# Performance work log

Hardware: AMD Instinct MI355X
Metric: run time of the kernel (lower is better)

The kernel has to match this reference:

```python
import jax, jax.numpy as jnp
import numpy as np

VOCAB, D_MODEL, N_STATE, H_HEADS, LAYERS = 64, 512, 32, 16, 4
EXPAND = 2
D_INNER = EXPAND * D_MODEL          # 1024
P_HEAD = D_INNER // H_HEADS         # 64
CONV_DIM = D_INNER + 2 * N_STATE    # x, B, C share the depthwise conv
K_CONV = 4
D_IN_PROJ = 2 * D_INNER + 2 * N_STATE + H_HEADS  # z, x, B, C, dt
BATCH, SEQ = 4, 1024
EPS = 1e-5


def rmsnorm(x, w):
    return x * jax.lax.rsqrt(jnp.mean(x * x, axis=-1, keepdims=True) + EPS) * w


def silu(x):
    return x * jax.nn.sigmoid(x)


def causal_depthwise_conv(x, w, b):
    # x: [B,L,C], w: [C,K], b: [C]; causal (left) padding, depthwise groups
    xt = jnp.transpose(x, (0, 2, 1))  # [B,C,L]
    out = jax.lax.conv_general_dilated(xt, w[:, None, :], (1,), [(K_CONV - 1, 0)], feature_group_count=w.shape[0])
    return jnp.transpose(out, (0, 2, 1)) + b


def ssd(xh, dt, A, Bm, Cm, Dp):
    # Mamba2 SSD recurrence. xh [B,L,H,P], dt [B,L,H], A [H], Bm/Cm [B,L,N], Dp [H]
    dA = jnp.exp(dt * A)              # decay per (batch, step, head)
    dtx = dt[..., None] * xh          # [B,L,H,P]

    def step(h, inp):
        dA_t, dtx_t, B_t, C_t = inp
        # h: [B,H,P,N]
        h = dA_t[:, :, None, None] * h + dtx_t[..., None] * B_t[:, None, None, :]
        y = jnp.einsum('bhpn,bn->bhp', h, C_t)
        return h, y

    h0 = jnp.zeros((xh.shape[0], H_HEADS, P_HEAD, N_STATE), xh.dtype)
    _, ys = jax.lax.scan(step, h0, (jnp.moveaxis(dA, 1, 0), jnp.moveaxis(dtx, 1, 0), jnp.moveaxis(Bm, 1, 0), jnp.moveaxis(Cm, 1, 0)))
    return jnp.moveaxis(ys, 0, 1) + xh * Dp[None, None, :, None]


def mamba_block(x, norm_w, W_in, b_in, conv_w, conv_b, dt_bias, A_log, Dp, gnorm_w, W_out, b_out):
    res = x
    u = rmsnorm(x, norm_w)
    zxbcdt = u @ W_in + b_in                                # [B,L,D_IN_PROJ]
    z = zxbcdt[..., :D_INNER]
    xBC = zxbcdt[..., D_INNER:D_INNER + CONV_DIM]
    dt = zxbcdt[..., D_INNER + CONV_DIM:]                   # [B,L,H]
    xBC = silu(causal_depthwise_conv(xBC, conv_w, conv_b))
    xc = xBC[..., :D_INNER]
    Bm = xBC[..., D_INNER:D_INNER + N_STATE]
    Cm = xBC[..., D_INNER + N_STATE:]
    dt = jax.nn.softplus(dt + dt_bias)
    xh = xc.reshape(xc.shape[0], xc.shape[1], H_HEADS, P_HEAD)
    y = ssd(xh, dt, -jnp.exp(A_log), Bm, Cm, Dp)
    y = y.reshape(y.shape[0], y.shape[1], D_INNER)
    y = rmsnorm(y * silu(z), gnorm_w)                       # gated RMSNorm
    return res + y @ W_out + b_out


def forward(input_tokens, emb, norm_w, W_in, b_in, conv_w, conv_b, dt_bias, A_log, D_param, gnorm_w, W_out, b_out, head_w, head_b):
    h = emb[input_tokens]
    for i in range(LAYERS):
        h = mamba_block(h, norm_w[i], W_in[i], b_in[i], conv_w[i], conv_b[i], dt_bias[i], A_log[i], D_param[i], gnorm_w[i], W_out[i], b_out[i])
    return h @ head_w + head_b


def setup_inputs() -> dict:
    key = jax.random.key(0)
    ks = jax.random.split(key, 8)
    s = 0.02
    return {
        'input_tokens': jax.random.randint(ks[0], (BATCH, SEQ), 0, VOCAB),
        'emb': jax.random.normal(ks[1], (VOCAB, D_MODEL), jnp.float32) * s,
        'norm_w': jnp.ones((LAYERS, D_MODEL), jnp.float32),
        'W_in': jax.random.normal(ks[2], (LAYERS, D_MODEL, D_IN_PROJ), jnp.float32) * s,
        'b_in': jnp.zeros((LAYERS, D_IN_PROJ), jnp.float32),
        'conv_w': jax.random.normal(ks[3], (LAYERS, CONV_DIM, K_CONV), jnp.float32) * 0.1,
        'conv_b': jnp.zeros((LAYERS, CONV_DIM), jnp.float32),
        'dt_bias': jnp.tile(jnp.log(jnp.expm1(jnp.linspace(0.001, 0.1, H_HEADS, dtype=jnp.float32))), (LAYERS, 1)),
        'A_log': jnp.tile(jnp.log(jnp.arange(1, H_HEADS + 1, dtype=jnp.float32)), (LAYERS, 1)),
        'D_param': jnp.ones((LAYERS, H_HEADS), jnp.float32),
        'gnorm_w': jnp.ones((LAYERS, D_INNER), jnp.float32),
        'W_out': jax.random.normal(ks[4], (LAYERS, D_INNER, D_MODEL), jnp.float32) * s,
        'b_out': jnp.zeros((LAYERS, D_MODEL), jnp.float32),
        'head_w': jax.random.normal(ks[5], (D_MODEL, VOCAB), jnp.float32) * s,
        'head_b': jnp.zeros((VOCAB,), jnp.float32),
    }


def reference(input_tokens, emb, norm_w, W_in, b_in, conv_w, conv_b, dt_bias, A_log, D_param, gnorm_w, W_out, b_out, head_w, head_b):
    return forward(input_tokens, emb, norm_w, W_in, b_in, conv_w, conv_b, dt_bias, A_log, D_param, gnorm_w, W_out, b_out, head_w, head_b)
```

## Files before the change

### kernel.cpp

```cpp
#include <hip/hip_runtime.h>
#include <hip/hip_bf16.h>

#define VOCAB     64
#define D_MODEL   512
#define N_STATE   32
#define H_HEADS   16
#define LAYERS    4
#define D_INNER   1024
#define P_HEAD    64
#define CONV_DIM  1088
#define K_CONV    4
#define D_IN_PROJ 2128
#define NPAD_IN   2176
#define NPAD_HEAD 64
#define BATCH     4
#define SEQ       1024
#define NTOK      (BATCH*SEQ)
#define EPS       1e-5f
#define CL        64
#define NC        (SEQ/CL)
#define PSTR      80

typedef __bf16 bf16x8 __attribute__((ext_vector_type(8)));
typedef float  f32x4  __attribute__((ext_vector_type(4)));

__device__ __forceinline__ float sigmoidf_(float x) { return 1.f / (1.f + __expf(-x)); }
__device__ __forceinline__ float softplusf_(float x) { return (x > 20.f) ? x : log1pf(__expf(x)); }

__device__ __forceinline__ void gload_lds16(const void* g, void* l) {
  __builtin_amdgcn_global_load_lds((const __attribute__((address_space(1))) void*)g,
                                   (__attribute__((address_space(3))) void*)l,
                                   16, 0, 0);
}

__global__ void rmsnorm512_kernel(const float* __restrict__ x, const float* __restrict__ w,
                                  __bf16* __restrict__ out,
                                  const int* __restrict__ tok, const float* __restrict__ emb,
                                  float* __restrict__ hout) {
  int tokid = blockIdx.x;
  int tid = threadIdx.x;
  float v0, v1;
  if (tok) {
    const float* er = emb + (size_t)tok[tokid] * D_MODEL;
    v0 = er[tid]; v1 = er[tid + 256];
    float* hr = hout + (size_t)tokid * D_MODEL;
    hr[tid] = v0; hr[tid + 256] = v1;
  } else {
    const float* xr = x + (size_t)tokid * D_MODEL;
    v0 = xr[tid]; v1 = xr[tid + 256];
  }
  float ss = v0 * v0 + v1 * v1;
  #pragma unroll
  for (int o = 32; o >= 1; o >>= 1) ss += __shfl_xor(ss, o);
  __shared__ float red[4];
  if ((tid & 63) == 0) red[tid >> 6] = ss;
  __syncthreads();
  float tot = red[0] + red[1] + red[2] + red[3];
  float sc = rsqrtf(tot * (1.f / D_MODEL) + EPS);
  out[(size_t)tokid * D_MODEL + tid]       = (__bf16)(v0 * sc * w[tid]);
  out[(size_t)tokid * D_MODEL + tid + 256] = (__bf16)(v1 * sc * w[tid + 256]);
}

__global__ void transpose_cast_kernel(const float* __restrict__ W, __bf16* __restrict__ Wt,
                                      int K, int N, int Npad) {
  W  += (size_t)blockIdx.z * K * N;
  Wt += (size_t)blockIdx.z * Npad * K;
  __shared__ float T[32][33];
  int n0 = blockIdx.x * 32, k0 = blockIdx.y * 32;
  int tx = threadIdx.x & 31, ty = threadIdx.x >> 5;
  #pragma unroll
  for (int i = 0; i < 4; i++) {
    int n = n0 + tx;
    T[ty + i * 8][tx] = (n < N) ? W[(size_t)(k0 + ty + i * 8) * N + n] : 0.f;
  }
  __syncthreads();
  #pragma unroll
  for (int i = 0; i < 4; i++)
    Wt[(size_t)(n0 + ty + i * 8) * K + k0 + tx] = (__bf16)T[tx][ty + i * 8];
}

#define TK 64
__global__ __launch_bounds__(256) void gemm_bf16_kernel(
    const __bf16* __restrict__ A, const __bf16* __restrict__ Bt,
    const float* __restrict__ bias, const float* __restrict__ res,
    float* __restrict__ C, __bf16* __restrict__ Cbf, int K, int N, int ldc) {
  __shared__ __bf16 As[64 * TK];
  __shared__ __bf16 Bs[64 * TK];
  int tid = threadIdx.x;
  int lane = tid & 63, wave = tid >> 6;
  int wm = wave >> 1, wn = wave & 1;
  int q = lane >> 4, l16 = lane & 15;
  size_t row0 = (size_t)blockIdx.y * 64;
  int col0 = blockIdx.x * 64;
  const __bf16* Ab = A + row0 * K;
  const __bf16* Bb = Bt + (size_t)col0 * K;

  f32x4 acc[2][2];
  #pragma unroll
  for (int i = 0; i < 2; i++)
    #pragma unroll
    for (int j = 0; j < 2; j++) acc[i][j] = (f32x4){0.f, 0.f, 0.f, 0.f};

  for (int k0 = 0; k0 < K; k0 += TK) {
    #pragma unroll
    for (int r = 0; r < 2; r++) {
      int lin = r * 256 + tid;
      size_t goff = (size_t)(lin >> 3) * K + k0 + (lin & 7) * 8;
      gload_lds16(Ab + goff, As + lin * 8);
      gload_lds16(Bb + goff, Bs + lin * 8);
    }
    __syncthreads();
    #pragma unroll
    for (int ks = 0; ks < 2; ks++) {
      bf16x8 af[2], bfv[2];
      #pragma unroll
      for (int i = 0; i < 2; i++)
        af[i] = *(const bf16x8*)(As + (wm * 32 + i * 16 + l16) * TK + ks * 32 + q * 8);
      #pragma unroll
      for (int j = 0; j < 2; j++)
        bfv[j] = *(const bf16x8*)(Bs + (wn * 32 + j * 16 + l16) * TK + ks * 32 + q * 8);
      #pragma unroll
      for (int i = 0; i < 2; i++)
        #pragma unroll
        for (int j = 0; j < 2; j++)
          acc[i][j] = __builtin_amdgcn_mfma_f32_16x16x32_bf16(af[i], bfv[j], acc[i][j], 0, 0, 0);
    }
    __syncthreads();
  }

  #pragma unroll
  for (int i = 0; i < 2; i++) {
    size_t mrow = row0 + wm * 32 + i * 16 + q * 4;
    #pragma unroll
    for (int j = 0; j < 2; j++) {
      int col = col0 + wn * 32 + j * 16 + l16;
      if (col < N) {
        float bv = bias ? bias[col] : 0.f;
        #pragma unroll
        for (int rr = 0; rr < 4; rr++) {
          size_t off = (mrow + rr) * (size_t)ldc + col;
          float v = acc[i][j][rr] + bv;
          if (res) v += res[off];
          if (C)   C[off] = v;
          if (Cbf) Cbf[off] = (__bf16)v;
        }
      }
    }
  }
}

__global__ __launch_bounds__(256) void gemm_bf16_128(
    const __bf16* __restrict__ A, const __bf16* __restrict__ Bt,
    const float* __restrict__ bias, __bf16* __restrict__ Cbf,
    int K, int N, int ldc) {
  __shared__ __bf16 As[128 * TK];
  __shared__ __bf16 Bs[128 * TK];
  int tid = threadIdx.x;
  int lane = tid & 63, wave = tid >> 6;
  int wm = wave >> 1, wn = wave & 1;
  int q = lane >> 4, l16 = lane & 15;
  size_t row0 = (size_t)blockIdx.y * 128;
  int col0 = blockIdx.x * 128;
  const __bf16* Ab = A + row0 * K;
  const __bf16* Bb = Bt + (size_t)col0 * K;

  f32x4 acc[4][4];
  #pragma unroll
  for (int i = 0; i < 4; i++)
    #pragma unroll
    for (int j = 0; j < 4; j++) acc[i][j] = (f32x4){0.f, 0.f, 0.f, 0.f};

  for (int k0 = 0; k0 < K; k0 += TK) {
    #pragma unroll
    for (int r = 0; r < 4; r++) {
      int lin = r * 256 + tid;
      size_t goff = (size_t)(lin >> 3) * K + k0 + (lin & 7) * 8;
      gload_lds16(Ab + goff, As + lin * 8);
      gload_lds16(Bb + goff, Bs + lin * 8);
    }
    __syncthreads();
    #pragma unroll
    for (int ks = 0; ks < 2; ks++) {
      bf16x8 af[4], bfv[4];
      #pragma unroll
      for (int i = 0; i < 4; i++)
        af[i] = *(const bf16x8*)(As + (wm * 64 + i * 16 + l16) * TK + ks * 32 + q * 8);
      #pragma unroll
      for (int j = 0; j < 4; j++)
        bfv[j] = *(const bf16x8*)(Bs + (wn * 64 + j * 16 + l16) * TK + ks * 32 + q * 8);
      #pragma unroll
      for (int i = 0; i < 4; i++)
        #pragma unroll
        for (int j = 0; j < 4; j++)
          acc[i][j] = __builtin_amdgcn_mfma_f32_16x16x32_bf16(af[i], bfv[j], acc[i][j], 0, 0, 0);
    }
    __syncthreads();
  }

  #pragma unroll
  for (int i = 0; i < 4; i++) {
    size_t mrow = row0 + wm * 64 + i * 16 + q * 4;
    #pragma unroll
    for (int j = 0; j < 4; j++) {
      int col = col0 + wn * 64 + j * 16 + l16;
      if (col < N) {
        float bv = bias[col];
        #pragma unroll
        for (int rr = 0; rr < 4; rr++)
          Cbf[(mrow + rr) * (size_t)ldc + col] = (__bf16)(acc[i][j][rr] + bv);
      }
    }
  }
}

__device__ __forceinline__ void wave0_dt_cumsum(
    const __bf16* __restrict__ zxbf, const float* __restrict__ dt_bias,
    int b, int h, int t0, int tid, float* ldt, float* lcs) {
  if (tid < 64) {
    float dv = (float)zxbf[((size_t)(b * SEQ + t0 + tid)) * D_IN_PROJ + 2 * D_INNER + 2 * N_STATE + h]
               + dt_bias[h];
    float dtv = softplusf_(dv);
    float cs = dtv;
    #pragma unroll
    for (int off = 1; off < 64; off <<= 1) {
      float o = __shfl_up(cs, off);
      if (tid >= off) cs += o;
    }
    ldt[tid] = dtv;
    lcs[tid] = cs;
  }
}

__global__ __launch_bounds__(256) void ssd_local_kernel(
    const __bf16* __restrict__ zxbf, const float* __restrict__ conv_w,
    const float* __restrict__ conv_b, const float* __restrict__ dt_bias,
    const float* __restrict__ A_log,
    float* __restrict__ Slocal, float* __restrict__ dAprod) {
  int blk = blockIdx.x;
  int c = blk % NC;
  int h = (blk / NC) % H_HEADS;
  int b = blk / (NC * H_HEADS);
  int tid = threadIdx.x;
  int lane = tid & 63, wave = tid >> 6;
  int q = lane >> 4, l16 = lane & 15;
  int t0 = c * CL;
  float A = -__expf(A_log[h]);
  __shared__ __bf16 rawx[68][64];
  __shared__ __bf16 rawB[68][32];
  __shared__ __bf16 lxT[64][PSTR];
  __shared__ __bf16 lBT[32][PSTR];
  __shared__ float ldt[64], lcs[64];
  for (int i = tid; i < 68 * 8; i += 256) {
    int r = i >> 3, c0 = (i & 7) * 8;
    int gr = t0 - 3 + r;
    bf16x8 v;
    #pragma unroll
    for (int k = 0; k < 8; k++) v[k] = (__bf16)0.f;
    if (gr >= 0)
      v = *(const bf16x8*)(zxbf + ((size_t)(b * SEQ + gr)) * D_IN_PROJ + D_INNER + h * 64 + c0);
    *(bf16x8*)(&rawx[r][c0]) = v;
  }
  for (int i = tid; i < 68 * 4; i += 256) {
    int r = i >> 2, c0 = (i & 3) * 8;
    int gr = t0 - 3 + r;
    bf16x8 v;
    #pragma unroll
    for (int k = 0; k < 8; k++) v[k] = (__bf16)0.f;
    if (gr >= 0)
      v = *(const bf16x8*)(zxbf + ((size_t)(b * SEQ + gr)) * D_IN_PROJ + 2 * D_INNER + c0);
    *(bf16x8*)(&rawB[r][c0]) = v;
  }
  wave0_dt_cumsum(zxbf, dt_bias, b, h, t0, tid, ldt, lcs);
  __syncthreads();
  float cs63 = lcs[63];
  {
    int p = tid & 63;
    const float* w = conv_w + (h * 64 + p) * K_CONV;
    float w0 = w[0], w1 = w[1], w2 = w[2], w3 = w[3];
    float cb = conv_b[h * 64 + p];
    for (int i = tid; i < CL * 64; i += 256) {
      int t = i >> 6;
      float a = cb + w0 * (float)rawx[t][p] + w1 * (float)rawx[t + 1][p]
                   + w2 * (float)rawx[t + 2][p] + w3 * (float)rawx[t + 3][p];
      lxT[p][t] = (__bf16)(a * sigmoidf_(a));
    }
  }
  {
    int n = tid & 31;
    const float* w = conv_w + (D_INNER + n) * K_CONV;
    float w0 = w[0], w1 = w[1], w2 = w[2], w3 = w[3];
    float cb = conv_b[D_INNER + n];
    for (int i = tid; i < CL * 32; i += 256) {
      int t = i >> 5;
      float a = cb + w0 * (float)rawB[t][n] + w1 * (float)rawB[t + 1][n]
                   + w2 * (float)rawB[t + 2][n] + w3 * (float)rawB[t + 3][n];
      float v = a * sigmoidf_(a);
      float wt = ldt[t] * __expf(A * (cs63 - lcs[t]));
      lBT[n][t] = (__bf16)(v * wt);
    }
  }
  __syncthreads();
  f32x4 acc[2];
  acc[0] = (f32x4){0.f,0.f,0.f,0.f}; acc[1] = (f32x4){0.f,0.f,0.f,0.f};
  #pragma unroll
  for (int kb = 0; kb < 2; kb++) {
    bf16x8 af = *(const bf16x8*)(&lxT[wave * 16 + l16][kb * 32 + q * 8]);
    #pragma unroll
    for (int j = 0; j < 2; j++) {
      bf16x8 bf = *(const bf16x8*)(&lBT[l16 + 16 * j][kb * 32 + q * 8]);
      acc[j] = __builtin_amdgcn_mfma_f32_16x16x32_bf16(af, bf, acc[j], 0, 0, 0);
    }
  }
  float* dst = Slocal + (size_t)blk * 2048;
  #pragma unroll
  for (int j = 0; j < 2; j++) {
    int n = l16 + 16 * j;
    #pragma unroll
    for (int rr = 0; rr < 4; rr++) {
      int p = wave * 16 + q * 4 + rr;
      dst[p * 32 + n] = acc[j][rr];
    }
  }
  if (tid == 0) dAprod[blk] = __expf(A * cs63);
}

__global__ __launch_bounds__(256) void ssd_out_kernel(
    const __bf16* __restrict__ zxbf, const float* __restrict__ conv_w,
    const float* __restrict__ conv_b, const float* __restrict__ dt_bias,
    const float* __restrict__ A_log, const float* __restrict__ Dp,
    const float* __restrict__ Slocal, const float* __restrict__ dAprod,
    __bf16* __restrict__ y) {
  int blk = blockIdx.x;
  int c = blk % NC;
  int h = (blk / NC) % H_HEADS;
  int b = blk / (NC * H_HEADS);
  int tid = threadIdx.x;
  int lane = tid & 63, wave = tid >> 6;
  int q = lane >> 4, l16 = lane & 15;
  int t0 = c * CL;
  float A = -__expf(A_log[h]);
  float D = Dp[h];
  __shared__ __bf16 rawbuf[2 * 68 * 64];
  __shared__ __bf16 lxT[64][PSTR];
  __shared__ __bf16 lB[64][32];
  __shared__ __bf16 lC[64][32];
  __shared__ __bf16 lS[64][32];
  __shared__ float ldt[64], lcs[64];
  __shared__ float pr[NC];
  __bf16* rawx = rawbuf;
  __bf16* rawBC = rawbuf + 68 * 64;
  for (int i = tid; i < 68 * 8; i += 256) {
    int r = i >> 3, c0 = (i & 7) * 8;
    int gr = t0 - 3 + r;
    bf16x8 vx, vbc;
    #pragma unroll
    for (int k = 0; k < 8; k++) { vx[k] = (__bf16)0.f; vbc[k] = (__bf16)0.f; }
    if (gr >= 0) {
      const __bf16* rowp = zxbf + ((size_t)(b * SEQ + gr)) * D_IN_PROJ;
      vx  = *(const bf16x8*)(rowp + D_INNER + h * 64 + c0);
      vbc = *(const bf16x8*)(rowp + 2 * D_INNER + c0);
    }
    *(bf16x8*)(rawx + r * 64 + c0)  = vx;
    *(bf16x8*)(rawBC + r * 64 + c0) = vbc;
  }
  if (tid < NC) pr[tid] = dAprod[(blk - c) + tid];
  wave0_dt_cumsum(zxbf, dt_bias, b, h, t0, tid, ldt, lcs);
  __syncthreads();
  {
    int p = tid & 63;
    const float* w = conv_w + (h * 64 + p) * K_CONV;
    float w0 = w[0], w1 = w[1], w2 = w[2], w3 = w[3];
    float cb = conv_b[h * 64 + p];
    for (int i = tid; i < CL * 64; i += 256) {
      int t = i >> 6;
      float a = cb + w0 * (float)rawx[t * 64 + p] + w1 * (float)rawx[(t + 1) * 64 + p]
                   + w2 * (float)rawx[(t + 2) * 64 + p] + w3 * (float)rawx[(t + 3) * 64 + p];
      lxT[p][t] = (__bf16)(a * sigmoidf_(a));
    }
  }
  {
    int col = tid & 63;
    const float* w = conv_w + (D_INNER + col) * K_CONV;
    float w0 = w[0], w1 = w[1], w2 = w[2], w3 = w[3];
    float cb = conv_b[D_INNER + col];
    for (int i = tid; i < CL * 64; i += 256) {
      int t = i >> 6;
      float a = cb + w0 * (float)rawBC[t * 64 + col] + w1 * (float)rawBC[(t + 1) * 64 + col]
                   + w2 * (float)rawBC[(t + 2) * 64 + col] + w3 * (float)rawBC[(t + 3) * 64 + col];
      float v = a * sigmoidf_(a);
      if (col < 32) lB[t][col] = (__bf16)v; else lC[t][col - 32] = (__bf16)v;
    }
  }
  {
    int p = tid >> 2, n0 = (tid & 3) * 8;
    const float* sl = Slocal + (size_t)(blk - c) * 2048 + p * 32 + n0;
    float st[8] = {};
    for (int j = 0; j < c; j++) {
      f32x4 a = *(const f32x4*)(sl + (size_t)j * 2048);
      f32x4 bq = *(const f32x4*)(sl + (size_t)j * 2048 + 4);
      float prj = pr[j];
      #pragma unroll
      for (int k = 0; k < 4; k++) { st[k] = prj * st[k] + a[k]; st[4 + k] = prj * st[4 + k] + bq[k]; }
    }
    #pragma unroll
    for (int k = 0; k < 8; k++) lS[p][n0 + k] = (__bf16)st[k];
  }
  __syncthreads();
  bf16x8 afC = *(const bf16x8*)(&lC[wave * 16 + l16][q * 8]);
  f32x4 accG[4], accI[4], accY[4];
  #pragma unroll
  for (int j = 0; j < 4; j++) {
    accG[j] = (f32x4){0.f,0.f,0.f,0.f};
    accI[j] = (f32x4){0.f,0.f,0.f,0.f};
    accY[j] = (f32x4){0.f,0.f,0.f,0.f};
  }
  #pragma unroll
  for (int j = 0; j < 4; j++) {
    bf16x8 bf = *(const bf16x8*)(&lB[l16 + 16 * j][q * 8]);
    accG[j] = __builtin_amdgcn_mfma_f32_16x16x32_bf16(afC, bf, accG[j], 0, 0, 0);
  }
  #pragma unroll
  for (int j = 0; j < 4; j++) {
    bf16x8 bf = *(const bf16x8*)(&lS[l16 + 16 * j][q * 8]);
    accI[j] = __builtin_amdgcn_mfma_f32_16x16x32_bf16(afC, bf, accI[j], 0, 0, 0);
  }
  __bf16* pP = rawbuf + wave * 16 * PSTR;
  #pragma unroll
  for (int j = 0; j < 4; j++) {
    int s = l16 + 16 * j;
    float css = lcs[s], dts = ldt[s];
    #pragma unroll
    for (int rr = 0; rr < 4; rr++) {
      int tl = q * 4 + rr;
      int t = wave * 16 + tl;
      float val = accG[j][rr] * __expf(A * (lcs[t] - css)) * dts;
      if (s == t) val += D;
      if (s > t) val = 0.f;
      pP[tl * PSTR + s] = (__bf16)val;
    }
  }
  #pragma unroll
  for (int kb = 0; kb < 2; kb++) {
    bf16x8 afP = *(const bf16x8*)(pP + l16 * PSTR + kb * 32 + q * 8);
    #pragma unroll
    for (int j = 0; j < 4; j++) {
      bf16x8 bf = *(const bf16x8*)(&lxT[l16 + 16 * j][kb * 32 + q * 8]);
      accY[j] = __builtin_amdgcn_mfma_f32_16x16x32_bf16(afP, bf, accY[j], 0, 0, 0);
    }
  }
  #pragma unroll
  for (int rr = 0; rr < 4; rr++) {
    int t = wave * 16 + q * 4 + rr;
    float cumt = __expf(A * lcs[t]);
    __bf16* yrow = y + ((size_t)(b * SEQ + t0 + t)) * D_INNER + h * 64;
    #pragma unroll
    for (int j = 0; j < 4; j++) {
      int p = l16 + 16 * j;
      yrow[p] = (__bf16)(accY[j][rr] + cumt * accI[j][rr]);
    }
  }
}

__global__ void gate_norm_kernel(const __bf16* __restrict__ zxbf, const float* __restrict__ gw,
                                 const __bf16* __restrict__ y, __bf16* __restrict__ ybf) {
  int tok = blockIdx.x;
  int tid = threadIdx.x;
  const __bf16* zr = zxbf + (size_t)tok * D_IN_PROJ;
  const __bf16* yr = y + (size_t)tok * D_INNER;
  float v[4];
  float ss = 0.f;
  #pragma unroll
  for (int i = 0; i < 4; i++) {
    int d = tid + i * 256;
    float z = (float)zr[d];
    float g = (float)yr[d] * z * sigmoidf_(z);
    v[i] = g;
    ss += g * g;
  }
  #pragma unroll
  for (int o = 32; o >= 1; o >>= 1) ss += __shfl_xor(ss, o);
  __shared__ float red[4];
  if ((tid & 63) == 0) red[tid >> 6] = ss;
  __syncthreads();
  float tot = red[0] + red[1] + red[2] + red[3];
  float sc = rsqrtf(tot * (1.f / D_INNER) + EPS);
  #pragma unroll
  for (int i = 0; i < 4; i++) {
    int d = tid + i * 256;
    ybf[(size_t)tok * D_INNER + d] = (__bf16)(v[i] * sc * gw[d]);
  }
}

extern "C" void kernel_launch(void* const* d_in, const int* in_sizes, int n_in,
                              void* d_out, int out_size, void* d_ws, size_t ws_size,
                              hipStream_t stream) {
  const int*   tok     = (const int*)  d_in[0];
  const float* emb     = (const float*)d_in[1];
  const float* norm_w  = (const float*)d_in[2];
  const float* W_in    = (const float*)d_in[3];
  const float* b_in    = (const float*)d_in[4];
  const float* conv_w  = (const float*)d_in[5];
  const float* conv_b  = (const float*)d_in[6];
  const float* dt_bias = (const float*)d_in[7];
  const float* A_log   = (const float*)d_in[8];
  const float* D_par   = (const float*)d_in[9];
  const float* gnorm_w = (const float*)d_in[10];
  const float* W_out   = (const float*)d_in[11];
  const float* b_out   = (const float*)d_in[12];
  const float* head_w  = (const float*)d_in[13];
  const float* head_b  = (const float*)d_in[14];
  float* out = (float*)d_out;

  char* p = (char*)d_ws;
  auto alloc = [&](size_t bytes) { void* r = (void*)p; p += (bytes + 255) & ~(size_t)255; return r; };
  float*  h      = (float*) alloc((size_t)NTOK * D_MODEL * 4);
  float*  slocal = (float*) alloc((size_t)BATCH * H_HEADS * NC * P_HEAD * N_STATE * 4);
  float*  daprod = (float*) alloc((size_t)BATCH * H_HEADS * NC * 4);
  __bf16* y      = (__bf16*)alloc((size_t)NTOK * D_INNER * 2);
  __bf16* zxbf   = (__bf16*)alloc((size_t)NTOK * D_IN_PROJ * 2);
  __bf16* ubf    = (__bf16*)alloc((size_t)NTOK * D_MODEL * 2);
  __bf16* ybf    = (__bf16*)alloc((size_t)NTOK * D_INNER * 2);
  __bf16* hbf    = (__bf16*)alloc((size_t)NTOK * D_MODEL * 2);
  __bf16* WtIn   = (__bf16*)alloc((size_t)LAYERS * NPAD_IN * D_MODEL * 2);
  __bf16* WtOut  = (__bf16*)alloc((size_t)LAYERS * D_MODEL * D_INNER * 2);
  __bf16* WtHead = (__bf16*)alloc((size_t)NPAD_HEAD * D_MODEL * 2);

  transpose_cast_kernel<<<dim3(NPAD_IN / 32, D_MODEL / 32, LAYERS), 256, 0, stream>>>(
      W_in, WtIn, D_MODEL, D_IN_PROJ, NPAD_IN);
  transpose_cast_kernel<<<dim3(D_MODEL / 32, D_INNER / 32, LAYERS), 256, 0, stream>>>(
      W_out, WtOut, D_INNER, D_MODEL, D_MODEL);
  transpose_cast_kernel<<<dim3(NPAD_HEAD / 32, D_MODEL / 32, 1), 256, 0, stream>>>(
      head_w, WtHead, D_MODEL, VOCAB, NPAD_HEAD);

  for (int l = 0; l < LAYERS; l++) {
    rmsnorm512_kernel<<<NTOK, 256, 0, stream>>>(
        h, norm_w + (size_t)l * D_MODEL, ubf,
        (l == 0) ? tok : nullptr, (l == 0) ? emb : nullptr, h);

    gemm_bf16_128<<<dim3(NPAD_IN / 128, NTOK / 128), 256, 0, stream>>>(
        ubf, WtIn + (size_t)l * NPAD_IN * D_MODEL, b_in + (size_t)l * D_IN_PROJ,
        zxbf, D_MODEL, D_IN_PROJ, D_IN_PROJ);

    ssd_local_kernel<<<BATCH * H_HEADS * NC, 256, 0, stream>>>(
        zxbf, conv_w + (size_t)l * CONV_DIM * K_CONV, conv_b + (size_t)l * CONV_DIM,
        dt_bias + (size_t)l * H_HEADS, A_log + (size_t)l * H_HEADS, slocal, daprod);
    ssd_out_kernel<<<BATCH * H_HEADS * NC, 256, 0, stream>>>(
        zxbf, conv_w + (size_t)l * CONV_DIM * K_CONV, conv_b + (size_t)l * CONV_DIM,
        dt_bias + (size_t)l * H_HEADS, A_log + (size_t)l * H_HEADS,
        D_par + (size_t)l * H_HEADS, slocal, daprod, y);

    gate_norm_kernel<<<NTOK, 256, 0, stream>>>(zxbf, gnorm_w + (size_t)l * D_INNER, y, ybf);

    gemm_bf16_kernel<<<dim3(D_MODEL / 64, NTOK / 64), 256, 0, stream>>>(
        ybf, WtOut + (size_t)l * D_MODEL * D_INNER, b_out + (size_t)l * D_MODEL, h, h,
        (l == LAYERS - 1) ? hbf : nullptr, D_INNER, D_MODEL, D_MODEL);
  }

  gemm_bf16_kernel<<<dim3(NPAD_HEAD / 64, NTOK / 64), 256, 0, stream>>>(
      hbf, WtHead, head_b, nullptr, out, nullptr, D_MODEL, VOCAB, VOCAB);
}
```

Baseline: 490.0 us.

## Vectorize norms per-wave, merge weight transposes, stage SSD outputs through LDS

The RMSNorm and gated-norm kernels now give one token to each wave and use 16-byte vector loads and stores, which removes the cross-wave LDS reduction and the barrier. The three weight transpose launches are merged into a single launch that decodes block indices. In the SSD local and out kernels, results are staged through reused LDS so each global store of Slocal and y is coalesced and vectorized. Together these target memory-access efficiency and launch overhead, at the cost of an extra barrier and more LDS traffic in the SSD kernels.

Result: no change. 489.4 us (-0.1%).

```diff
diff --git a/kernel.cpp b/kernel.cpp
--- a/kernel.cpp
+++ b/kernel.cpp
@@ -33,40 +33,63 @@
                                    16, 0, 0);
 }
 
-__global__ void rmsnorm512_kernel(const float* __restrict__ x, const float* __restrict__ w,
-                                  __bf16* __restrict__ out,
-                                  const int* __restrict__ tok, const float* __restrict__ emb,
-                                  float* __restrict__ hout) {
-  int tokid = blockIdx.x;
-  int tid = threadIdx.x;
-  float v0, v1;
+__global__ __launch_bounds__(256) void rmsnorm512_kernel(
+    const float* __restrict__ x, const float* __restrict__ w,
+    __bf16* __restrict__ out,
+    const int* __restrict__ tok, const float* __restrict__ emb,
+    float* __restrict__ hout) {
+  int wv = threadIdx.x >> 6, lane = threadIdx.x & 63;
+  int tokid = blockIdx.x * 4 + wv;
+  const float* src = tok ? emb + (size_t)tok[tokid] * D_MODEL
+                         : x + (size_t)tokid * D_MODEL;
+  f32x4 v0 = *(const f32x4*)(src + lane * 8);
+  f32x4 v1 = *(const f32x4*)(src + lane * 8 + 4);
   if (tok) {
-    const float* er = emb + (size_t)tok[tokid] * D_MODEL;
-    v0 = er[tid]; v1 = er[tid + 256];
     float* hr = hout + (size_t)tokid * D_MODEL;
-    hr[tid] = v0; hr[tid + 256] = v1;
+    *(f32x4*)(hr + lane * 8) = v0;
+    *(f32x4*)(hr + lane * 8 + 4) = v1;
+  }
+  float ss = v0[0]*v0[0] + v0[1]*v0[1] + v0[2]*v0[2] + v0[3]*v0[3]
+           + v1[0]*v1[0] + v1[1]*v1[1] + v1[2]*v1[2] + v1[3]*v1[3];
+  #pragma unroll
+  for (int o = 32; o >= 1; o >>= 1) ss += __shfl_xor(ss, o);
+  float sc = rsqrtf(ss * (1.f / D_MODEL) + EPS);
+  f32x4 w0 = *(const f32x4*)(w + lane * 8);
+  f32x4 w1 = *(const f32x4*)(w + lane * 8 + 4);
+  bf16x8 o8;
+  #pragma unroll
+  for (int k = 0; k < 4; k++) o8[k]     = (__bf16)(v0[k] * sc * w0[k]);
+  #pragma unroll
+  for (int k = 0; k < 4; k++) o8[4 + k] = (__bf16)(v1[k] * sc * w1[k]);
+  *(bf16x8*)(out + (size_t)tokid * D_MODEL + lane * 8) = o8;
+}
+
+__global__ __launch_bounds__(256) void transpose_all_kernel(
+    const float* __restrict__ W_in, const float* __restrict__ W_out,
+    const float* __restrict__ head_w,
+    __bf16* __restrict__ WtIn, __bf16* __restrict__ WtOut, __bf16* __restrict__ WtHead) {
+  int b = blockIdx.x;
+  const float* W; __bf16* Wt; int K, N, Npad, bx, by;
+  if (b < 4352) {
+    int z = b / 1088, r = b % 1088;
+    bx = r % 68; by = r / 68;
+    W = W_in + (size_t)z * D_MODEL * D_IN_PROJ;
+    Wt = WtIn + (size_t)z * NPAD_IN * D_MODEL;
+    K = D_MODEL; N = D_IN_PROJ; Npad = NPAD_IN;
+  } else if (b < 6400) {
+    int r = b - 4352; int z = r / 512; r %= 512;
+    bx = r % 16; by = r / 16;
+    W = W_out + (size_t)z * D_INNER * D_MODEL;
+    Wt = WtOut + (size_t)z * D_MODEL * D_INNER;
+    K = D_INNER; N = D_MODEL; Npad = D_MODEL;
   } else {
-    const float* xr = x + (size_t)tokid * D_MODEL;
-    v0 = xr[tid]; v1 = xr[tid + 256];
-  }
-  float ss = v0 * v0 + v1 * v1;
-  #pragma unroll
-  for (int o = 32; o >= 1; o >>= 1) ss += __shfl_xor(ss, o);
-  __shared__ float red[4];
-  if ((tid & 63) == 0) red[tid >> 6] = ss;
-  __syncthreads();
-  float tot = red[0] + red[1] + red[2] + red[3];
-  float sc = rsqrtf(tot * (1.f / D_MODEL) + EPS);
-  out[(size_t)tokid * D_MODEL + tid]       = (__bf16)(v0 * sc * w[tid]);
-  out[(size_t)tokid * D_MODEL + tid + 256] = (__bf16)(v1 * sc * w[tid + 256]);
-}
-
-__global__ void transpose_cast_kernel(const float* __restrict__ W, __bf16* __restrict__ Wt,
-                                      int K, int N, int Npad) {
-  W  += (size_t)blockIdx.z * K * N;
-  Wt += (size_t)blockIdx.z * Npad * K;
+    int r = b - 6400;
+    bx = r % 2; by = r / 2;
+    W = head_w; Wt = WtHead;
+    K = D_MODEL; N = VOCAB; Npad = NPAD_HEAD;
+  }
   __shared__ float T[32][33];
-  int n0 = blockIdx.x * 32, k0 = blockIdx.y * 32;
+  int n0 = bx * 32, k0 = by * 32;
   int tx = threadIdx.x & 31, ty = threadIdx.x >> 5;
   #pragma unroll
   for (int i = 0; i < 4; i++) {
@@ -245,11 +268,12 @@
   int q = lane >> 4, l16 = lane & 15;
   int t0 = c * CL;
   float A = -__expf(A_log[h]);
-  __shared__ __bf16 rawx[68][64];
-  __shared__ __bf16 rawB[68][32];
+  __shared__ __bf16 rawbuf[68 * 64 + 68 * 32];
   __shared__ __bf16 lxT[64][PSTR];
   __shared__ __bf16 lBT[32][PSTR];
   __shared__ float ldt[64], lcs[64];
+  __bf16* rawx = rawbuf;
+  __bf16* rawB = rawbuf + 68 * 64;
   for (int i = tid; i < 68 * 8; i += 256) {
     int r = i >> 3, c0 = (i & 7) * 8;
     int gr = t0 - 3 + r;
@@ -258,7 +282,7 @@
     for (int k = 0; k < 8; k++) v[k] = (__bf16)0.f;
     if (gr >= 0)
       v = *(const bf16x8*)(zxbf + ((size_t)(b * SEQ + gr)) * D_IN_PROJ + D_INNER + h * 64 + c0);
-    *(bf16x8*)(&rawx[r][c0]) = v;
+    *(bf16x8*)(rawx + r * 64 + c0) = v;
   }
   for (int i = tid; i < 68 * 4; i += 256) {
     int r = i >> 2, c0 = (i & 3) * 8;
@@ -268,7 +292,7 @@
     for (int k = 0; k < 8; k++) v[k] = (__bf16)0.f;
     if (gr >= 0)
       v = *(const bf16x8*)(zxbf + ((size_t)(b * SEQ + gr)) * D_IN_PROJ + 2 * D_INNER + c0);
-    *(bf16x8*)(&rawB[r][c0]) = v;
+    *(bf16x8*)(rawB + r * 32 + c0) = v;
   }
   wave0_dt_cumsum(zxbf, dt_bias, b, h, t0, tid, ldt, lcs);
   __syncthreads();
@@ -280,8 +304,8 @@
     float cb = conv_b[h * 64 + p];
     for (int i = tid; i < CL * 64; i += 256) {
       int t = i >> 6;
-      float a = cb + w0 * (float)rawx[t][p] + w1 * (float)rawx[t + 1][p]
-                   + w2 * (float)rawx[t + 2][p] + w3 * (float)rawx[t + 3][p];
+      float a = cb + w0 * (float)rawx[t * 64 + p] + w1 * (float)rawx[(t + 1) * 64 + p]
+                   + w2 * (float)rawx[(t + 2) * 64 + p] + w3 * (float)rawx[(t + 3) * 64 + p];
       lxT[p][t] = (__bf16)(a * sigmoidf_(a));
     }
   }
@@ -292,8 +316,8 @@
     float cb = conv_b[D_INNER + n];
     for (int i = tid; i < CL * 32; i += 256) {
       int t = i >> 5;
-      float a = cb + w0 * (float)rawB[t][n] + w1 * (float)rawB[t + 1][n]
-                   + w2 * (float)rawB[t + 2][n] + w3 * (float)rawB[t + 3][n];
+      float a = cb + w0 * (float)rawB[t * 32 + n] + w1 * (float)rawB[(t + 1) * 32 + n]
+                   + w2 * (float)rawB[(t + 2) * 32 + n] + w3 * (float)rawB[(t + 3) * 32 + n];
       float v = a * sigmoidf_(a);
       float wt = ldt[t] * __expf(A * (cs63 - lcs[t]));
       lBT[n][t] = (__bf16)(v * wt);
@@ -311,15 +335,23 @@
       acc[j] = __builtin_amdgcn_mfma_f32_16x16x32_bf16(af, bf, acc[j], 0, 0, 0);
     }
   }
-  float* dst = Slocal + (size_t)blk * 2048;
+  float* sT = (float*)rawbuf;
   #pragma unroll
   for (int j = 0; j < 2; j++) {
     int n = l16 + 16 * j;
     #pragma unroll
     for (int rr = 0; rr < 4; rr++) {
       int p = wave * 16 + q * 4 + rr;
-      dst[p * 32 + n] = acc[j][rr];
-    }
+      sT[p * 36 + n] = acc[j][rr];
+    }
+  }
+  {
+    int row = tid >> 2, c0 = (tid & 3) * 8;
+    f32x4 a = *(const f32x4*)(sT + row * 36 + c0);
+    f32x4 b2 = *(const f32x4*)(sT + row * 36 + c0 + 4);
+    float* dstp = Slocal + (size_t)blk * 2048 + row * 32 + c0;
+    *(f32x4*)dstp = a;
+    *(f32x4*)(dstp + 4) = b2;
   }
   if (tid == 0) dAprod[blk] = __expf(A * cs63);
 }
@@ -448,47 +480,72 @@
       accY[j] = __builtin_amdgcn_mfma_f32_16x16x32_bf16(afP, bf, accY[j], 0, 0, 0);
     }
   }
+  __syncthreads();
+  __bf16* yT = rawbuf;
   #pragma unroll
   for (int rr = 0; rr < 4; rr++) {
     int t = wave * 16 + q * 4 + rr;
     float cumt = __expf(A * lcs[t]);
-    __bf16* yrow = y + ((size_t)(b * SEQ + t0 + t)) * D_INNER + h * 64;
     #pragma unroll
     for (int j = 0; j < 4; j++) {
       int p = l16 + 16 * j;
-      yrow[p] = (__bf16)(accY[j][rr] + cumt * accI[j][rr]);
-    }
-  }
-}
-
-__global__ void gate_norm_kernel(const __bf16* __restrict__ zxbf, const float* __restrict__ gw,
-                                 const __bf16* __restrict__ y, __bf16* __restrict__ ybf) {
-  int tok = blockIdx.x;
-  int tid = threadIdx.x;
-  const __bf16* zr = zxbf + (size_t)tok * D_IN_PROJ;
-  const __bf16* yr = y + (size_t)tok * D_INNER;
-  float v[4];
+      yT[t * 72 + p] = (__bf16)(accY[j][rr] + cumt * accI[j][rr]);
+    }
+  }
+  {
+    int row = tid >> 2, col0 = (tid & 3) * 16;
+    bf16x8 o0 = *(const bf16x8*)(yT + row * 72 + col0);
+    bf16x8 o1 = *(const bf16x8*)(yT + row * 72 + col0 + 8);
+    __bf16* yrow = y + ((size_t)(b * SEQ + t0 + row)) * D_INNER + h * 64 + col0;
+    *(bf16x8*)yrow = o0;
+    *(bf16x8*)(yrow + 8) = o1;
+  }
+}
+
+__global__ __launch_bounds__(256) void gate_norm_kernel(
+    const __bf16* __restrict__ zxbf, const float* __restrict__ gw,
+    const __bf16* __restrict__ y, __bf16* __restrict__ ybf) {
+  int wv = threadIdx.x >> 6, lane = threadIdx.x & 63;
+  int tokid = blockIdx.x * 4 + wv;
+  const __bf16* zr = zxbf + (size_t)tokid * D_IN_PROJ + lane * 16;
+  const __bf16* yr = y + (size_t)tokid * D_INNER + lane * 16;
+  bf16x8 z0 = *(const bf16x8*)zr;
+  bf16x8 z1 = *(const bf16x8*)(zr + 8);
+  bf16x8 y0 = *(const bf16x8*)yr;
+  bf16x8 y1 = *(const bf16x8*)(yr + 8);
+  float g[16];
   float ss = 0.f;
   #pragma unroll
-  for (int i = 0; i < 4; i++) {
-    int d = tid + i * 256;
-    float z = (float)zr[d];
-    float g = (float)yr[d] * z * sigmoidf_(z);
-    v[i] = g;
-    ss += g * g;
+  for (int k = 0; k < 8; k++) {
+    float zz = (float)z0[k];
+    float gg = (float)y0[k] * zz * sigmoidf_(zz);
+    g[k] = gg; ss += gg * gg;
+  }
+  #pragma unroll
+  for (int k = 0; k < 8; k++) {
+    float zz = (float)z1[k];
+    float gg = (float)y1[k] * zz * sigmoidf_(zz);
+    g[8 + k] = gg; ss += gg * gg;
   }
   #pragma unroll
   for (int o = 32; o >= 1; o >>= 1) ss += __shfl_xor(ss, o);
-  __shared__ float red[4];
-  if ((tid & 63) == 0) red[tid >> 6] = ss;
-  __syncthreads();
-  float tot = red[0] + red[1] + red[2] + red[3];
-  float sc = rsqrtf(tot * (1.f / D_INNER) + EPS);
-  #pragma unroll
-  for (int i = 0; i < 4; i++) {
-    int d = tid + i * 256;
-    ybf[(size_t)tok * D_INNER + d] = (__bf16)(v[i] * sc * gw[d]);
-  }
+  float sc = rsqrtf(ss * (1.f / D_INNER) + EPS);
+  f32x4 w0 = *(const f32x4*)(gw + lane * 16);
+  f32x4 w1 = *(const f32x4*)(gw + lane * 16 + 4);
+  f32x4 w2 = *(const f32x4*)(gw + lane * 16 + 8);
+  f32x4 w3 = *(const f32x4*)(gw + lane * 16 + 12);
+  bf16x8 o0, o1;
+  #pragma unroll
+  for (int k = 0; k < 4; k++) o0[k]     = (__bf16)(g[k]      * sc * w0[k]);
+  #pragma unroll
+  for (int k = 0; k < 4; k++) o0[4 + k] = (__bf16)(g[4 + k]  * sc * w1[k]);
+  #pragma unroll
+  for (int k = 0; k < 4; k++) o1[k]     = (__bf16)(g[8 + k]  * sc * w2[k]);
+  #pragma unroll
+  for (int k = 0; k < 4; k++) o1[4 + k] = (__bf16)(g[12 + k] * sc * w3[k]);
+  __bf16* orow = ybf + (size_t)tokid * D_INNER + lane * 16;
+  *(bf16x8*)orow = o0;
+  *(bf16x8*)(orow + 8) = o1;
 }
 
 extern "C" void kernel_launch(void* const* d_in, const int* in_sizes, int n_in,
@@ -525,15 +582,10 @@
   __bf16* WtOut  = (__bf16*)alloc((size_t)LAYERS * D_MODEL * D_INNER * 2);
   __bf16* WtHead = (__bf16*)alloc((size_t)NPAD_HEAD * D_MODEL * 2);
 
-  transpose_cast_kernel<<<dim3(NPAD_IN / 32, D_MODEL / 32, LAYERS), 256, 0, stream>>>(
-      W_in, WtIn, D_MODEL, D_IN_PROJ, NPAD_IN);
-  transpose_cast_kernel<<<dim3(D_MODEL / 32, D_INNER / 32, LAYERS), 256, 0, stream>>>(
-      W_out, WtOut, D_INNER, D_MODEL, D_MODEL);
-  transpose_cast_kernel<<<dim3(NPAD_HEAD / 32, D_MODEL / 32, 1), 256, 0, stream>>>(
-      head_w, WtHead, D_MODEL, VOCAB, NPAD_HEAD);
+  transpose_all_kernel<<<6432, 256, 0, stream>>>(W_in, W_out, head_w, WtIn, WtOut, WtHead);
 
   for (int l = 0; l < LAYERS; l++) {
-    rmsnorm512_kernel<<<NTOK, 256, 0, stream>>>(
+    rmsnorm512_kernel<<<NTOK / 4, 256, 0, stream>>>(
         h, norm_w + (size_t)l * D_MODEL, ubf,
         (l == 0) ? tok : nullptr, (l == 0) ? emb : nullptr, h);
 
@@ -549,7 +601,7 @@
         dt_bias + (size_t)l * H_HEADS, A_log + (size_t)l * H_HEADS,
         D_par + (size_t)l * H_HEADS, slocal, daprod, y);
 
-    gate_norm_kernel<<<NTOK, 256, 0, stream>>>(zxbf, gnorm_w + (size_t)l * D_INNER, y, ybf);
+    gate_norm_kernel<<<NTOK / 4, 256, 0, stream>>>(zxbf, gnorm_w + (size_t)l * D_INNER, y, ybf);
 
     gemm_bf16_kernel<<<dim3(D_MODEL / 64, NTOK / 64), 256, 0, stream>>>(
         ybf, WtOut + (size_t)l * D_MODEL * D_INNER, b_out + (size_t)l * D_MODEL, h, h,
```
